# Kernel optimization log

Hardware: AMD Instinct MI355X
Metric: run time of the kernel (lower is better)

The kernel has to match this reference:

```python
import jax, jax.numpy as jnp
import numpy as np

IMG_W, IMG_H = 800, 800
OH, OW = 7, 7


def setup_inputs() -> dict:
    key = jax.random.key(0)
    k1, k2, k3 = jax.random.split(key, 3)
    feature_map = jax.random.normal(k1, (1, 256, 200, 200), dtype=jnp.float32)
    # boxes in image pixel coords, x1<=x2 and y1<=y2
    xs = jnp.sort(jax.random.uniform(k2, (1024, 2), dtype=jnp.float32) * (IMG_W - 1), axis=1)
    ys = jnp.sort(jax.random.uniform(k3, (1024, 2), dtype=jnp.float32) * (IMG_H - 1), axis=1)
    boxes = jnp.stack([xs[:, 0], ys[:, 0], xs[:, 1], ys[:, 1]], axis=1)
    return {"feature_map": feature_map, "boxes": boxes}


def reference(feature_map, boxes):
    # feature_map: [1, C, H, W]; boxes: [N, 4] (x1, y1, x2, y2) in image coords
    fm = feature_map[0]                      # [C, H, W]
    C, H, W = fm.shape
    scale = jnp.array([W / IMG_W, H / IMG_H, W / IMG_W, H / IMG_H], dtype=boxes.dtype)
    b = jnp.floor(boxes * scale).astype(jnp.int32)
    x1 = jnp.clip(b[:, 0], 0, W - 1)
    y1 = jnp.clip(b[:, 1], 0, H - 1)
    x2 = jnp.clip(b[:, 2] + 1, x1 + 1, W)    # exclusive end, clamped like torch slicing
    y2 = jnp.clip(b[:, 3] + 1, y1 + 1, H)
    rh = y2 - y1                             # [N]
    rw = x2 - x1
    # adaptive_avg_pool2d bin edges: start=floor(i*L/O), end=ceil((i+1)*L/O)
    i = jnp.arange(OH)
    j = jnp.arange(OW)
    rs = y1[:, None] + (i[None, :] * rh[:, None]) // OH                  # [N, OH]
    re = y1[:, None] + ((i[None, :] + 1) * rh[:, None] + OH - 1) // OH
    cs = x1[:, None] + (j[None, :] * rw[:, None]) // OW                  # [N, OW]
    ce = x1[:, None] + ((j[None, :] + 1) * rw[:, None] + OW - 1) // OW
    # integral image with zero row/col padding: ii[c, r, k] = sum fm[c, :r, :k]
    ii = jnp.pad(jnp.cumsum(jnp.cumsum(fm, axis=1), axis=2), ((0, 0), (1, 0), (1, 0)))

    def S(r, c):  # r: [N, OH], c: [N, OW] -> [N, C, OH, OW]
        return ii[:, r[:, :, None], c[:, None, :]].transpose(1, 0, 2, 3)

    total = S(re, ce) - S(rs, ce) - S(re, cs) + S(rs, cs)               # [N, C, OH, OW]
    area = ((re - rs)[:, :, None] * (ce - cs)[:, None, :]).astype(fm.dtype)  # [N, OH, OW]
    return total / area[:, None, :, :]
```

## Files before the change

kernel.cpp:

```cpp
#include <hip/hip_runtime.h>

#define C_CH  256
#define H_FM  200
#define W_FM  200
#define N_BOX 1024
#define OHp   7
#define OWp   7
#define NG    16
#define CG    16
#define CGP   17
#define NCHUNK 25
#define CHROWS 8
#define GSTRIDE (H_FM * W_FM * CG)
#define HSTRIDE (W_FM * CG)
#define AUXG    (NCHUNK * HSTRIDE)
#define GPAD  17
#define TW    40
#define NWT   5


__global__ __launch_bounds__(256) void fused_scan_kernel(const float* __restrict__ fm,
                                                         float* __restrict__ T2) {
    __shared__ float tile[CHROWS][TW][CGP];
    const int t  = threadIdx.x;
    const int ch = blockIdx.x;
    const int g  = blockIdx.y;
    const int h0 = ch * CHROWS;
    const float* fmg = fm + (size_t)(g * CG) * (H_FM * W_FM) + (size_t)h0 * W_FM;

    const float* gp[5];
    int lo[5];
    #pragma unroll
    for (int s = 0; s < 5; ++s) {
        int f   = s * 256 + t;
        int ci  = f / 80;
        int rem = f - ci * 80;
        int r   = rem / 10;
        int w4  = rem - r * 10;
        gp[s] = fmg + (size_t)ci * (H_FM * W_FM) + r * W_FM + w4 * 4;
        lo[s] = (r * TW + w4 * 4) * CGP + (ci ^ w4);
    }

    const int cg = t & 15;
    const int rr = t >> 4;
    float accw = 0.0f;
    float4 stage[5];

    #pragma unroll
    for (int s = 0; s < 5; ++s) stage[s] = *(const float4*)(gp[s]);

    for (int wt = 0; wt < NWT; ++wt) {
        #pragma unroll
        for (int s = 0; s < 5; ++s) {
            float4 v = stage[s];
            float* p = &tile[0][0][0] + lo[s];
            p[0]       = v.x;
            p[CGP]     = v.y;
            p[2 * CGP] = v.z;
            p[3 * CGP] = v.w;
        }
        __syncthreads();

        if (wt + 1 < NWT) {
            #pragma unroll
            for (int s = 0; s < 5; ++s)
                stage[s] = *(const float4*)(gp[s] + (wt + 1) * TW);
        }

        if (t < CHROWS * CG) {
            #pragma unroll
            for (int w = 0; w < TW; ++w) {
                accw += tile[rr][w][cg ^ (w >> 2)];
                tile[rr][w][cg ^ (w >> 2)] = accw;
            }
        }
        __syncthreads();

        float* dstT = T2 + (size_t)g * GSTRIDE;
        #pragma unroll
        for (int k = 0; k < 3; ++k) {
            int col = k * 256 + t;
            if (col < TW * CG) {
                int w   = col >> 4;
                int cc  = col & 15;
                int ccs = cc ^ (w >> 2);
                float vacc = 0.0f;
                float* dcol = dstT + (size_t)(wt * TW + w) * CG + cc;
                #pragma unroll
                for (int r = 0; r < CHROWS; ++r) {
                    vacc += tile[r][w][ccs];
                    dcol[(size_t)(h0 + r) * HSTRIDE] = vacc;
                }
            }
        }
        __syncthreads();
    }
}

__global__ __launch_bounds__(64) void aux_scan_kernel(const float* __restrict__ T2,
                                                      float* __restrict__ aux2) {
    const int idx = blockIdx.x * 64 + threadIdx.x;
    const int g   = idx / (HSTRIDE / 4);
    const int r4  = idx - g * (HSTRIDE / 4);
    const float4* tp = (const float4*)T2 + (size_t)g * (GSTRIDE / 4)
                                         + (size_t)(CHROWS - 1) * (HSTRIDE / 4) + r4;
    float4* ap = (float4*)aux2 + (size_t)g * (AUXG / 4) + r4;
    float4 acc = make_float4(0.f, 0.f, 0.f, 0.f);
    #pragma unroll
    for (int cq = 0; cq < NCHUNK; ++cq) {
        float4 v = tp[(size_t)cq * (CHROWS * HSTRIDE / 4)];
        ap[(size_t)cq * (HSTRIDE / 4)] = acc;
        acc.x += v.x; acc.y += v.y; acc.z += v.z; acc.w += v.w;
    }
}

__global__ __launch_bounds__(256) void pool8_kernel(const float* __restrict__ T2,
                                                    const float* __restrict__ aux2,
                                                    const float* __restrict__ boxes,
                                                    float* __restrict__ out) {
    __shared__ float grid[196][GPAD];
    __shared__ int er[14];
    __shared__ int ec[14];
    __shared__ float rcpA[49];
    const int bx   = blockIdx.x;
    const int half = bx >> 13;
    const int wi   = bx & 8191;
    const int n    = wi >> 3;
    const int g    = (wi & 7) + half * 8;
    const int t    = threadIdx.x;

    const float4 box = ((const float4*)boxes)[n];
    int b0 = (int)floorf(box.x * 0.25f);
    int b1 = (int)floorf(box.y * 0.25f);
    int b2 = (int)floorf(box.z * 0.25f);
    int b3 = (int)floorf(box.w * 0.25f);
    int x1 = min(max(b0, 0), W_FM - 1);
    int y1 = min(max(b1, 0), H_FM - 1);
    int x2 = min(max(b2 + 1, x1 + 1), W_FM);
    int y2 = min(max(b3 + 1, y1 + 1), H_FM);
    int rh = y2 - y1;
    int rw = x2 - x1;

    if (t < 14) {
        er[t] = (t < 7) ? (y1 + (t * rh) / OHp)
                        : (y1 + ((t - 6) * rh + OHp - 1) / OHp);
    } else if (t >= 64 && t < 78) {
        int u = t - 64;
        ec[u] = (u < 7) ? (x1 + (u * rw) / OWp)
                        : (x1 + ((u - 6) * rw + OWp - 1) / OWp);
    }
    __syncthreads();

    if (t < 49) {
        int i = t / 7;
        int j = t - i * 7;
        rcpA[t] = 1.0f / (float)((er[7 + i] - er[i]) * (ec[7 + j] - ec[j]));
    }

    {
        const int c4 = t & 3;
        const int p0 = t >> 2;
        const float* Tg = T2   + (size_t)g * GSTRIDE + c4 * 4;
        const float* Ag = aux2 + (size_t)g * AUXG   + c4 * 4;
        #pragma unroll
        for (int it = 0; it < 4; ++it) {
            int pos = it * 64 + p0;
            if (pos < 196) {
                int ri = pos / 14;
                int ci = pos - ri * 14;
                int r = er[ri];
                int k = ec[ci];
                float4 v = make_float4(0.f, 0.f, 0.f, 0.f);
                if (r > 0 && k > 0) {
                    float4 tv = *(const float4*)(Tg + ((size_t)(r - 1) * W_FM + (k - 1)) * CG);
                    float4 av = *(const float4*)(Ag + ((size_t)((r - 1) >> 3) * W_FM + (k - 1)) * CG);
                    v.x = tv.x + av.x; v.y = tv.y + av.y;
                    v.z = tv.z + av.z; v.w = tv.w + av.w;
                }
                grid[pos][c4 * 4 + 0] = v.x;
                grid[pos][c4 * 4 + 1] = v.y;
                grid[pos][c4 * 4 + 2] = v.z;
                grid[pos][c4 * 4 + 3] = v.w;
            }
        }
    }
    __syncthreads();

    float* dst = out + (size_t)n * (C_CH * 49) + (size_t)g * (CG * 49);
    #pragma unroll
    for (int k = 0; k < 4; ++k) {
        int flat = k * 256 + t;
        if (flat < CG * 49) {
            int cg  = flat / 49;
            int rem = flat - cg * 49;
            int i = rem / 7;
            int j = rem - i * 7;
            float a = grid[(7 + i) * 14 + 7 + j][cg];
            float b = grid[i * 14 + 7 + j][cg];
            float c = grid[(7 + i) * 14 + j][cg];
            float d = grid[i * 14 + j][cg];
            dst[flat] = ((a - b) - (c - d)) * rcpA[rem];
        }
    }
}

__device__ __forceinline__ void box_edges(const float4 box, int i, int j,
                                          int& rs, int& re, int& cs, int& ce) {
    int b0 = (int)floorf(box.x * 0.25f);
    int b1 = (int)floorf(box.y * 0.25f);
    int b2 = (int)floorf(box.z * 0.25f);
    int b3 = (int)floorf(box.w * 0.25f);
    int x1 = min(max(b0, 0), W_FM - 1);
    int y1 = min(max(b1, 0), H_FM - 1);
    int x2 = min(max(b2 + 1, x1 + 1), W_FM);
    int y2 = min(max(b3 + 1, y1 + 1), H_FM);
    int rh = y2 - y1;
    int rw = x2 - x1;
    rs = y1 + (i * rh) / OHp;
    re = y1 + ((i + 1) * rh + OHp - 1) / OHp;
    cs = x1 + (j * rw) / OWp;
    ce = x1 + ((j + 1) * rw + OWp - 1) / OWp;
}

__global__ __launch_bounds__(256) void pool_direct_kernel(const float* __restrict__ fm,
                                                          const float* __restrict__ boxes,
                                                          float* __restrict__ out) {
    const int idx = blockIdx.x * 256 + threadIdx.x;
    const int j  = idx % OWp;
    const int t1 = idx / OWp;
    const int i  = t1 % OHp;
    const int t2 = t1 / OHp;
    const int c  = t2 % C_CH;
    const int n  = t2 / C_CH;

    const float4 box = ((const float4*)boxes)[n];
    int rs, re, cs, ce;
    box_edges(box, i, j, rs, re, cs, ce);

    const float* base = fm + (size_t)c * (H_FM * W_FM);
    float sum = 0.0f;
    for (int r = rs; r < re; ++r) {
        const float* rowp = base + (size_t)r * W_FM;
        for (int k = cs; k < ce; ++k) sum += rowp[k];
    }
    float area = (float)((re - rs) * (ce - cs));
    out[idx] = sum / area;
}

extern "C" void kernel_launch(void* const* d_in, const int* in_sizes, int n_in,
                              void* d_out, int out_size, void* d_ws, size_t ws_size,
                              hipStream_t stream) {
    const float* fm    = (const float*)d_in[0];
    const float* boxes = (const float*)d_in[1];
    float* out = (float*)d_out;

    const size_t tBytes   = (size_t)NG * GSTRIDE * sizeof(float);
    const size_t auxBytes = (size_t)NG * AUXG * sizeof(float);
    const int    total    = N_BOX * C_CH * OHp * OWp;
    const int    blocks   = total / 256;

    if (ws_size >= tBytes + auxBytes) {
        float* T2   = (float*)d_ws;
        float* aux2 = (float*)((char*)d_ws + tBytes);
        fused_scan_kernel<<<dim3(NCHUNK, NG), 256, 0, stream>>>(fm, T2);
        aux_scan_kernel<<<200, 64, 0, stream>>>(T2, aux2);
        pool8_kernel<<<N_BOX * NG, 256, 0, stream>>>(T2, aux2, boxes, out);
    } else {
        pool_direct_kernel<<<blocks, 256, 0, stream>>>(fm, boxes, out);
    }
}
```

Before: 131.7 us.

## Fold chunk-offset scan into pool kernel and vectorize column-scan stores

Removes the separate aux_scan kernel and its global aux buffer. Each pool block now loads the last-row partial sums of all 25 chunks for its 14 column edges into shared memory and does the prefix scan over chunks locally. The column-scan write in the first kernel is also switched from scalar to float4 stores, using 160 threads instead of up to three passes of 256. The trade is one fewer launch and global pass against about 350 extra gathered float4 loads and a serial 25-step scan in every one of 16384 pool blocks, plus more shared memory per block.

```diff
diff --git a/kernel.cpp b/kernel.cpp
--- a/kernel.cpp
+++ b/kernel.cpp
@@ -13,7 +13,6 @@
 #define CHROWS 8
 #define GSTRIDE (H_FM * W_FM * CG)
 #define HSTRIDE (W_FM * CG)
-#define AUXG    (NCHUNK * HSTRIDE)
 #define GPAD  17
 #define TW    40
 #define NWT   5
@@ -77,48 +76,30 @@
         __syncthreads();
 
         float* dstT = T2 + (size_t)g * GSTRIDE;
-        #pragma unroll
-        for (int k = 0; k < 3; ++k) {
-            int col = k * 256 + t;
-            if (col < TW * CG) {
-                int w   = col >> 4;
-                int cc  = col & 15;
-                int ccs = cc ^ (w >> 2);
-                float vacc = 0.0f;
-                float* dcol = dstT + (size_t)(wt * TW + w) * CG + cc;
-                #pragma unroll
-                for (int r = 0; r < CHROWS; ++r) {
-                    vacc += tile[r][w][ccs];
-                    dcol[(size_t)(h0 + r) * HSTRIDE] = vacc;
-                }
+        if (t < TW * CG / 4) {
+            int w  = t >> 2;
+            int c4 = t & 3;
+            int s  = w >> 2;
+            float4 vacc = make_float4(0.f, 0.f, 0.f, 0.f);
+            #pragma unroll
+            for (int r = 0; r < CHROWS; ++r) {
+                vacc.x += tile[r][w][(c4 * 4 + 0) ^ s];
+                vacc.y += tile[r][w][(c4 * 4 + 1) ^ s];
+                vacc.z += tile[r][w][(c4 * 4 + 2) ^ s];
+                vacc.w += tile[r][w][(c4 * 4 + 3) ^ s];
+                *(float4*)(dstT + (size_t)(h0 + r) * HSTRIDE
+                                + (size_t)(wt * TW + w) * CG + c4 * 4) = vacc;
             }
         }
         __syncthreads();
     }
 }
 
-__global__ __launch_bounds__(64) void aux_scan_kernel(const float* __restrict__ T2,
-                                                      float* __restrict__ aux2) {
-    const int idx = blockIdx.x * 64 + threadIdx.x;
-    const int g   = idx / (HSTRIDE / 4);
-    const int r4  = idx - g * (HSTRIDE / 4);
-    const float4* tp = (const float4*)T2 + (size_t)g * (GSTRIDE / 4)
-                                         + (size_t)(CHROWS - 1) * (HSTRIDE / 4) + r4;
-    float4* ap = (float4*)aux2 + (size_t)g * (AUXG / 4) + r4;
-    float4 acc = make_float4(0.f, 0.f, 0.f, 0.f);
-    #pragma unroll
-    for (int cq = 0; cq < NCHUNK; ++cq) {
-        float4 v = tp[(size_t)cq * (CHROWS * HSTRIDE / 4)];
-        ap[(size_t)cq * (HSTRIDE / 4)] = acc;
-        acc.x += v.x; acc.y += v.y; acc.z += v.z; acc.w += v.w;
-    }
-}
-
 __global__ __launch_bounds__(256) void pool8_kernel(const float* __restrict__ T2,
-                                                    const float* __restrict__ aux2,
                                                     const float* __restrict__ boxes,
                                                     float* __restrict__ out) {
     __shared__ float grid[196][GPAD];
+    __shared__ float auxL[NCHUNK][14][CG];
     __shared__ int er[14];
     __shared__ int ec[14];
     __shared__ float rcpA[49];
@@ -158,10 +139,43 @@
     }
 
     {
+        const float* Tg = T2 + (size_t)g * GSTRIDE;
+        #pragma unroll
+        for (int it = 0; it < 6; ++it) {
+            int f = it * 256 + t;
+            if (f < NCHUNK * 14 * 4) {
+                int q   = f / 56;
+                int rem = f - q * 56;
+                int ci  = rem >> 2;
+                int c4  = rem & 3;
+                int k   = ec[ci];
+                float4 v = make_float4(0.f, 0.f, 0.f, 0.f);
+                if (k > 0)
+                    v = *(const float4*)(Tg + (size_t)(q * CHROWS + CHROWS - 1) * HSTRIDE
+                                            + (size_t)(k - 1) * CG + c4 * 4);
+                ((float4*)&auxL[q][ci][0])[c4] = v;
+            }
+        }
+    }
+    __syncthreads();
+
+    if (t < 14 * CG) {
+        int ci  = t >> 4;
+        int chv = t & 15;
+        float acc = 0.0f;
+        #pragma unroll
+        for (int q = 0; q < NCHUNK; ++q) {
+            float v = auxL[q][ci][chv];
+            auxL[q][ci][chv] = acc;
+            acc += v;
+        }
+    }
+    __syncthreads();
+
+    {
         const int c4 = t & 3;
         const int p0 = t >> 2;
-        const float* Tg = T2   + (size_t)g * GSTRIDE + c4 * 4;
-        const float* Ag = aux2 + (size_t)g * AUXG   + c4 * 4;
+        const float* Tg = T2 + (size_t)g * GSTRIDE + c4 * 4;
         #pragma unroll
         for (int it = 0; it < 4; ++it) {
             int pos = it * 64 + p0;
@@ -173,7 +187,8 @@
                 float4 v = make_float4(0.f, 0.f, 0.f, 0.f);
                 if (r > 0 && k > 0) {
                     float4 tv = *(const float4*)(Tg + ((size_t)(r - 1) * W_FM + (k - 1)) * CG);
-                    float4 av = *(const float4*)(Ag + ((size_t)((r - 1) >> 3) * W_FM + (k - 1)) * CG);
+                    int cq = (r - 1) >> 3;
+                    float4 av = ((const float4*)&auxL[cq][ci][0])[c4];
                     v.x = tv.x + av.x; v.y = tv.y + av.y;
                     v.z = tv.z + av.z; v.w = tv.w + av.w;
                 }
@@ -254,17 +269,14 @@
     const float* boxes = (const float*)d_in[1];
     float* out = (float*)d_out;
 
-    const size_t tBytes   = (size_t)NG * GSTRIDE * sizeof(float);
-    const size_t auxBytes = (size_t)NG * AUXG * sizeof(float);
-    const int    total    = N_BOX * C_CH * OHp * OWp;
-    const int    blocks   = total / 256;
-
-    if (ws_size >= tBytes + auxBytes) {
-        float* T2   = (float*)d_ws;
-        float* aux2 = (float*)((char*)d_ws + tBytes);
+    const size_t tBytes = (size_t)NG * GSTRIDE * sizeof(float);
+    const int    total  = N_BOX * C_CH * OHp * OWp;
+    const int    blocks = total / 256;
+
+    if (ws_size >= tBytes) {
+        float* T2 = (float*)d_ws;
         fused_scan_kernel<<<dim3(NCHUNK, NG), 256, 0, stream>>>(fm, T2);
-        aux_scan_kernel<<<200, 64, 0, stream>>>(T2, aux2);
-        pool8_kernel<<<N_BOX * NG, 256, 0, stream>>>(T2, aux2, boxes, out);
+        pool8_kernel<<<N_BOX * NG, 256, 0, stream>>>(T2, boxes, out);
     } else {
         pool_direct_kernel<<<blocks, 256, 0, stream>>>(fm, boxes, out);
     }
```

Result: slower. 172.8 us (+31.2%).
